# Kernel optimization log

Hardware: AMD Instinct MI355X
Metric: run time of the kernel (lower is better)

Reference implementation:

```python
import jax, jax.numpy as jnp
import numpy as np
import math

N = 50000        # nodes
DEG = 16         # regular out-degree -> E = N*DEG edges, grouped by source node
B = 64           # graphs in batch
F = 128          # num_node_features
H = 128          # nhid == enhid
RATIO = 0.5      # edge_ratio
NUM_CONVS = 3
E = N * DEG


def setup_inputs() -> dict:
    key = jax.random.key(0)
    ks = jax.random.split(key, 18)
    s = 0.05
    x = jax.random.normal(ks[0], (N, F), jnp.float32)
    edge_src = jnp.repeat(jnp.arange(N, dtype=jnp.int32), DEG)          # sorted by src
    edge_dst = jax.random.randint(ks[1], (E,), 0, N, jnp.int32)
    batch = ((jnp.arange(N) * B) // N).astype(jnp.int32)                 # sorted graph ids
    edge_attr = jnp.ones((E, 1), jnp.float32)                            # edge_attr=None branch
    inp = {"x": x, "edge_attr": edge_attr, "edge_src": edge_src,
           "edge_dst": edge_dst, "batch": batch}
    # GCNConv weights: [F->H, H->H, H->H]
    inp["W_gcn0"] = jax.random.normal(ks[2], (F, H), jnp.float32) * s
    inp["b_gcn0"] = jnp.zeros((H,), jnp.float32)
    inp["W_gcn1"] = jax.random.normal(ks[3], (H, H), jnp.float32) * s
    inp["b_gcn1"] = jnp.zeros((H,), jnp.float32)
    inp["W_gcn2"] = jax.random.normal(ks[4], (H, H), jnp.float32) * s
    inp["b_gcn2"] = jnp.zeros((H,), jnp.float32)
    # EGNN edge convs: [1->H, H->H]
    inp["W_eg0"] = jax.random.normal(ks[5], (1, H), jnp.float32) * s
    inp["b_eg0"] = jnp.zeros((H,), jnp.float32)
    inp["W_eg1"] = jax.random.normal(ks[6], (H, H), jnp.float32) * s
    inp["b_eg1"] = jnp.zeros((H,), jnp.float32)
    # score convs: [H->1, H->1]
    inp["W_sc0"] = jax.random.normal(ks[7], (H, 1), jnp.float32) * s
    inp["b_sc0"] = jnp.zeros((1,), jnp.float32)
    inp["W_sc1"] = jax.random.normal(ks[8], (H, 1), jnp.float32) * s
    inp["b_sc1"] = jnp.zeros((1,), jnp.float32)
    return inp


def _gcn(x, src, dst, ew, W, b):
    # PyG GCNConv: add self-loops (weight 1), symmetric deg normalization, aggregate at dst.
    n = x.shape[0]
    loop = jnp.arange(n, dtype=src.dtype)
    src2 = jnp.concatenate([src, loop])
    dst2 = jnp.concatenate([dst, loop])
    ew2 = jnp.concatenate([ew, jnp.ones((n,), ew.dtype)])
    deg = jax.ops.segment_sum(ew2, dst2, n)
    dinv = jnp.where(deg > 0, jax.lax.rsqrt(jnp.maximum(deg, 1e-12)), 0.0)
    norm = dinv[src2] * dinv[dst2] * ew2                                  # [E+n]
    msg = (x @ W)[src2] * norm[:, None]                                    # gather + scale
    return jax.ops.segment_sum(msg, dst2, n) + b                           # scatter-add


def _egnn(e, src, W, b):
    # Edge conv: scatter edge features to their source node, gather back, linear map.
    agg = jax.ops.segment_sum(e, src, N)
    return agg[src] @ W + b


def _pool(h, batch):
    gmax = jax.ops.segment_max(h, batch, B)
    gsum = jax.ops.segment_sum(h, batch, B)
    cnt = jax.ops.segment_sum(jnp.ones((h.shape[0],), h.dtype), batch, B)
    gmean = gsum / cnt[:, None]
    return jnp.concatenate([gmax, gmean, gsum], axis=1)                    # [B, 3H]


def reference(x, edge_attr, edge_src, edge_dst, batch,
              W_gcn0, b_gcn0, W_gcn1, b_gcn1, W_gcn2, b_gcn2,
              W_eg0, b_eg0, W_eg1, b_eg1, W_sc0, b_sc0, W_sc1, b_sc1):
    gW = [W_gcn0, W_gcn1, W_gcn2]
    gb = [b_gcn0, b_gcn1, b_gcn2]
    eW = [W_eg0, W_eg1]
    eb = [b_eg0, b_eg1]
    sW = [W_sc0, W_sc1]
    sb = [b_sc0, b_sc1]
    src, dst = edge_src, edge_dst
    deg = DEG
    ew = jnp.ones((src.shape[0],), jnp.float32)
    h = x
    ea = edge_attr
    xs = jnp.zeros((B, 3 * H), jnp.float32)
    for i in range(NUM_CONVS):
        h = jax.nn.relu(_gcn(h, src, dst, ew, gW[i], gb[i]))
        if i < NUM_CONVS - 1:
            ea = jax.nn.relu(_egnn(ea, src, eW[i], eb[i]))
            score = jnp.tanh(_egnn(ea, src, sW[i], sb[i])[:, 0])           # [E_cur]
            k = math.ceil(RATIO * deg)                                      # per-src-node top-k
            vals, idx = jax.lax.top_k(score.reshape(N, deg), k)             # [N,k]
            dst = jnp.take_along_axis(dst.reshape(N, deg), idx, axis=1).reshape(-1)
            flat = (jnp.arange(N)[:, None] * deg + idx).reshape(-1)
            ea = ea[flat]
            src = jnp.repeat(jnp.arange(N, dtype=src.dtype), k)
            ew = jnp.clip(vals.reshape(-1), 0.0, 1.0)
            deg = k
        xs = xs + _pool(h, batch)
    return xs
```

## Files before the change

### kernel.cpp

```cpp
#include <hip/hip_runtime.h>
#include <math.h>

#define NNODES 50000
#define DEGREE 16
#define NGRAPH 64
#define CAP 64
#define LDA 136
#define NXCD 8
#define XRANGE (NNODES / NXCD)
#define NTILE 782

typedef unsigned short u16;
typedef unsigned int u32;
typedef unsigned long long u64;
using short8 = __attribute__((ext_vector_type(8))) short;
using f32x4  = __attribute__((ext_vector_type(4))) float;
using u16x4  = __attribute__((ext_vector_type(4))) unsigned short;

__device__ __forceinline__ u16 f2bf(float f) {
  union { float f; u32 u; } v; v.f = f;
  u32 u = v.u;
  return (u16)((u + 0x7FFFu + ((u >> 16) & 1u)) >> 16);
}
__device__ __forceinline__ float2 bf2x2(u32 u) {
  union { u32 u; float f; } lo, hi;
  lo.u = (u & 0xFFFFu) << 16; hi.u = u & 0xFFFF0000u;
  return make_float2(lo.f, hi.f);
}
__device__ __forceinline__ u32 pack2(float x, float y) {
  return (u32)f2bf(x) | ((u32)f2bf(y) << 16);
}
__device__ __forceinline__ int lowerb(const int* b, int n, int v) {
  int lo = 0, hi = n;
  while (lo < hi) { int m = (lo + hi) >> 1; if (b[m] < v) lo = m + 1; else hi = m; }
  return lo;
}

__global__ __launch_bounds__(256) void k_init(
    const float* __restrict__ eattr, const float* __restrict__ x,
    const float* __restrict__ weg, const float* __restrict__ beg,
    const float* __restrict__ wsc, const float* __restrict__ bsc,
    const float* __restrict__ W0, const float* __restrict__ W1,
    const float* __restrict__ W2, const float* __restrict__ W3,
    float* __restrict__ ew1, float* __restrict__ agg0,
    u16* __restrict__ xb, u16* __restrict__ Wt,
    const int* __restrict__ edst, int* __restrict__ cnt,
    int* __restrict__ slots) {
  int b = blockIdx.x, t = threadIdx.x;
  if (b < 6250) {
    int i = b * 256 + t;
    float4 v = reinterpret_cast<const float4*>(x)[i];
    u16x4 o = {f2bf(v.x), f2bf(v.y), f2bf(v.z), f2bf(v.w)};
    reinterpret_cast<u16x4*>(xb)[i] = o;
    if (i < NNODES) {
      const float4* p = reinterpret_cast<const float4*>(eattr + (size_t)i * DEGREE);
      float s = 0.f;
#pragma unroll
      for (int j = 0; j < 4; ++j) { float4 w = p[j]; s += w.x + w.y + w.z + w.w; }
      agg0[i] = s;
      float sc = 0.f;
      for (int k = 0; k < 128; ++k) {
        float e = fmaxf(fmaf(s, weg[k], beg[k]), 0.f);
        sc = fmaf(e, wsc[k], sc);
      }
      float v1 = tanhf(fmaf(16.f, sc, bsc[0]));
      ew1[i] = fminf(fmaxf(v1, 0.f), 1.f);
    }
  } else if (b < 6506) {
    int idx = (b - 6250) * 256 + t;
    int which = idx >> 14, r = idx & 16383;
    int k = r >> 7, n = r & 127;
    const float* W = which == 0 ? W0 : which == 1 ? W1 : which == 2 ? W2 : W3;
    Wt[which * 16384 + n * 128 + k] = f2bf(W[k * 128 + n]);
  } else {
    int kk = b - 6506;
    int r = kk & (NXCD - 1);
    int bi = kk >> 3;
    int rlo = r * XRANGE, rhi = rlo + XRANGE;
    int tid = bi * 256 + t;
    for (int e = tid; e < NNODES * DEGREE; e += 128 * 256) {
      int d = edst[e];
      if (d >= rlo && d < rhi) {
        int pos = atomicAdd(&cnt[d], 1);
        if (pos < CAP) slots[(size_t)d * CAP + pos] = e;
      }
    }
  }
}

__global__ __launch_bounds__(256) void k_gemmF(
    int nGemm, const u16* __restrict__ A, const u16* __restrict__ WtA,
    u16* __restrict__ outA,
    int nEg, const float* __restrict__ agg0, const float* __restrict__ weg,
    const float* __restrict__ beg, const u16* __restrict__ WtE,
    const float* __restrict__ beE, const float* __restrict__ wsc1,
    const float* __restrict__ bs1, float* __restrict__ ewOut) {
  __shared__ u16 Bs[128 * LDA];
  __shared__ u16 As[64 * LDA];
  int b = blockIdx.x, t = threadIdx.x;
  int eg = (b >= nGemm);
  const u16* Wsrc = eg ? WtE : WtA;
  for (int i = t; i < 2048; i += 256) {
    int r = i >> 4, c = (i & 15) << 3;
    *reinterpret_cast<uint4*>(&Bs[r * LDA + c]) =
        *reinterpret_cast<const uint4*>(&Wsrc[r * 128 + c]);
  }
  int m0 = (eg ? (b - nGemm) : b) * 64;
  if (eg) {
    for (int idx = t; idx < 64 * 128; idx += 256) {
      int r = idx >> 7, k = idx & 127;
      int row = m0 + r;
      float a = (row < NNODES) ? agg0[row] : 0.f;
      float v = 8.f * fmaxf(fmaf(a, weg[k], beg[k]), 0.f);
      As[r * LDA + k] = f2bf(v);
    }
  } else {
    for (int i = t; i < 1024; i += 256) {
      int r = i >> 4, c = (i & 15) << 3;
      int row = m0 + r;
      uint4 v = make_uint4(0u, 0u, 0u, 0u);
      if (row < NNODES) v = *reinterpret_cast<const uint4*>(&A[(size_t)row * 128 + c]);
      *reinterpret_cast<uint4*>(&As[r * LDA + c]) = v;
    }
  }
  __syncthreads();
  int wave = t >> 6, lane = t & 63;
  int lm = lane & 15, quad = lane >> 4;
  f32x4 z = {0.f, 0.f, 0.f, 0.f};
  f32x4 acc[8];
#pragma unroll
  for (int n = 0; n < 8; ++n) acc[n] = z;
  const u16* arow = &As[(wave * 16 + lm) * LDA + quad * 8];
#pragma unroll
  for (int kc = 0; kc < 4; ++kc) {
    short8 af = *reinterpret_cast<const short8*>(arow + kc * 32);
#pragma unroll
    for (int n = 0; n < 8; ++n) {
      short8 bf = *reinterpret_cast<const short8*>(
          &Bs[(n * 16 + lm) * LDA + kc * 32 + quad * 8]);
      acc[n] = __builtin_amdgcn_mfma_f32_16x16x32_bf16(af, bf, acc[n], 0, 0, 0);
    }
  }
  if (!eg) {
#pragma unroll
    for (int n = 0; n < 8; ++n) {
      int col = n * 16 + lm;
#pragma unroll
      for (int r = 0; r < 4; ++r) {
        int row = m0 + wave * 16 + quad * 4 + r;
        if (row < NNODES) outA[(size_t)row * 128 + col] = f2bf(acc[n][r]);
      }
    }
  } else {
    float s0 = 0.f, s1 = 0.f, s2 = 0.f, s3 = 0.f;
#pragma unroll
    for (int n = 0; n < 8; ++n) {
      int col = n * 16 + lm;
      float bb = beE[col], wv = wsc1[col];
      s0 = fmaf(fmaxf(acc[n][0] + bb, 0.f), wv, s0);
      s1 = fmaf(fmaxf(acc[n][1] + bb, 0.f), wv, s1);
      s2 = fmaf(fmaxf(acc[n][2] + bb, 0.f), wv, s2);
      s3 = fmaf(fmaxf(acc[n][3] + bb, 0.f), wv, s3);
    }
#pragma unroll
    for (int m = 8; m >= 1; m >>= 1) {
      s0 += __shfl_xor(s0, m, 64);
      s1 += __shfl_xor(s1, m, 64);
      s2 += __shfl_xor(s2, m, 64);
      s3 += __shfl_xor(s3, m, 64);
    }
    if (lm == 0) {
      float bsv = bs1[0];
      float sv[4] = {s0, s1, s2, s3};
#pragma unroll
      for (int r = 0; r < 4; ++r) {
        int row = m0 + wave * 16 + quad * 4 + r;
        if (row < NNODES) {
          float v = tanhf(fmaf(8.f, sv[r], bsv));
          ewOut[row] = fminf(fmaxf(v, 0.f), 1.f);
        }
      }
    }
  }
}

__global__ __launch_bounds__(256) void k_small(
    int nDinv, const int* __restrict__ cnt, const int* __restrict__ slots,
    const float* __restrict__ ewIn, float* __restrict__ dinv,
    float* __restrict__ wsrc, int keep,
    const u16* __restrict__ h, const int* __restrict__ batch,
    float* __restrict__ pmax, float* __restrict__ psum) {
  __shared__ float P[16 * 64];
  int b = blockIdx.x, t = threadIdx.x;
  if (b < nDinv) {
    int n = (b * 256 + t) >> 6;
    int lane = t & 63;
    if (n < NNODES) {
      int c = min(cnt[n], CAP);
      u32 ent = 0;
      if (lane < c) ent = (u32)slots[(size_t)n * CAP + lane];
      float e = (lane < c && (ent & 15u) < (u32)keep) ? ewIn[ent >> 4] : 0.f;
#pragma unroll
      for (int m = 32; m >= 1; m >>= 1) e += __shfl_xor(e, m, 64);
      float d = rsqrtf(1.0f + e);
      if (lane == 0) { dinv[n] = d; wsrc[n] = d * ewIn[n]; }
    }
  } else {
    int pb = b - nDinv;
    int g = pb >> 4, sl = pb & 15;
    int lo = lowerb(batch, NNODES, g);
    int hi = lowerb(batch, NNODES, g + 1);
    int len = hi - lo;
    int start = lo + (len * sl) / 16;
    int end = lo + (len * (sl + 1)) / 16;
    int lane = t & 63, rg = t >> 6;
    const u32* hb = reinterpret_cast<const u32*>(h);
    float mxx = 0.f, mxy = 0.f, smx = 0.f, smy = 0.f;
    for (int n = start + rg; n < end; n += 4) {
      float2 v = bf2x2(hb[(size_t)n * 64 + lane]);
      mxx = fmaxf(mxx, v.x); mxy = fmaxf(mxy, v.y);
      smx += v.x; smy += v.y;
    }
    P[(rg * 4 + 0) * 64 + lane] = mxx;
    P[(rg * 4 + 1) * 64 + lane] = mxy;
    P[(rg * 4 + 2) * 64 + lane] = smx;
    P[(rg * 4 + 3) * 64 + lane] = smy;
    __syncthreads();
    if (t < 64) {
      float amx = 0.f, amy = 0.f, asx = 0.f, asy = 0.f;
#pragma unroll
      for (int rgi = 0; rgi < 4; ++rgi) {
        amx = fmaxf(amx, P[(rgi * 4 + 0) * 64 + t]);
        amy = fmaxf(amy, P[(rgi * 4 + 1) * 64 + t]);
        asx += P[(rgi * 4 + 2) * 64 + t];
        asy += P[(rgi * 4 + 3) * 64 + t];
      }
      pmax[(size_t)pb * 128 + 2 * t]     = amx;
      pmax[(size_t)pb * 128 + 2 * t + 1] = amy;
      psum[(size_t)pb * 128 + 2 * t]     = asx;
      psum[(size_t)pb * 128 + 2 * t + 1] = asy;
    }
  }
}

__global__ __launch_bounds__(256) void k_aggp(
    int nAgg, const u16* __restrict__ xwb, const int* __restrict__ cnt,
    const int* __restrict__ slots, const float* __restrict__ wsrc,
    const float* __restrict__ dinv, const float* __restrict__ bias,
    u16* __restrict__ hout, int keep, int l0mode,
    const float* __restrict__ pmax, const float* __restrict__ psum,
    const int* __restrict__ batch, float* __restrict__ out, int poolAdd) {
  int b = blockIdx.x, t = threadIdx.x;
  if (b < nAgg) {
    int n = (b * 256 + t) >> 6;
    int lane = t & 63;
    if (n >= NNODES) return;
    int c = min(cnt[n], CAP);
    u32 e = 0;
    if (lane < c) e = (u32)slots[(size_t)n * CAP + lane];
    int kc; u32 ce;
    if (keep < 16) {
      bool valid = (lane < c) && ((e & 15u) < (u32)keep);
      u64 mask = __ballot(valid);
      kc = (int)__popcll(mask);
      u64 lt = ((u64)1 << lane) - 1;
      int pos = valid ? (int)__popcll(mask & lt) : 63 - (int)__popcll((~mask) & lt);
      ce = (u32)__builtin_amdgcn_ds_permute(pos << 2, (int)e);
    } else { kc = c; ce = e; }
    int sl = 0; float wl = 0.f;
    if (lane < kc) {
      sl = (int)(ce >> 4);
      wl = l0mode ? rsqrtf(1.0f + (float)min(cnt[sl], CAP)) : wsrc[sl];
    }
    const u32* base = reinterpret_cast<const u32*>(xwb);
    float2 acc = make_float2(0.f, 0.f);
    int i = 0;
    for (; i + 8 <= kc; i += 8) {
      u32 r[8]; float w[8];
#pragma unroll
      for (int j = 0; j < 8; ++j) {
        int s = __shfl(sl, i + j, 64);
        w[j] = __shfl(wl, i + j, 64);
        r[j] = base[(size_t)s * 64 + lane];
      }
#pragma unroll
      for (int j = 0; j < 8; ++j) {
        float2 v = bf2x2(r[j]);
        acc.x = fmaf(w[j], v.x, acc.x);
        acc.y = fmaf(w[j], v.y, acc.y);
      }
    }
    for (; i + 4 <= kc; i += 4) {
      u32 r[4]; float w[4];
#pragma unroll
      for (int j = 0; j < 4; ++j) {
        int s = __shfl(sl, i + j, 64);
        w[j] = __shfl(wl, i + j, 64);
        r[j] = base[(size_t)s * 64 + lane];
      }
#pragma unroll
      for (int j = 0; j < 4; ++j) {
        float2 v = bf2x2(r[j]);
        acc.x = fmaf(w[j], v.x, acc.x);
        acc.y = fmaf(w[j], v.y, acc.y);
      }
    }
    for (; i < kc; ++i) {
      int s = __shfl(sl, i, 64);
      float w = __shfl(wl, i, 64);
      float2 v = bf2x2(base[(size_t)s * 64 + lane]);
      acc.x = fmaf(w, v.x, acc.x);
      acc.y = fmaf(w, v.y, acc.y);
    }
    float di = l0mode ? rsqrtf(1.0f + (float)c) : dinv[n];
    float2 self = bf2x2(base[(size_t)n * 64 + lane]);
    float2 bv = reinterpret_cast<const float2*>(bias)[lane];
    float rx = fmaxf(fmaf(di, acc.x, fmaf(di * di, self.x, bv.x)), 0.f);
    float ry = fmaxf(fmaf(di, acc.y, fmaf(di * di, self.y, bv.y)), 0.f);
    reinterpret_cast<u32*>(hout + (size_t)n * 128)[lane] = pack2(rx, ry);
  } else {
    int g = b - nAgg;
    if (t >= 128) return;
    int f = t;
    float mx = 0.f, sm = 0.f;
    for (int s = 0; s < 16; ++s) {
      mx = fmaxf(mx, pmax[(size_t)(g * 16 + s) * 128 + f]);
      sm += psum[(size_t)(g * 16 + s) * 128 + f];
    }
    int lo = lowerb(batch, NNODES, g);
    int hi = lowerb(batch, NNODES, g + 1);
    float cf = (float)(hi - lo);
    float* og = out + g * 384;
    if (poolAdd) {
      og[f] += mx; og[128 + f] += sm / cf; og[256 + f] += sm;
    } else {
      og[f] = mx;  og[128 + f] = sm / cf;  og[256 + f] = sm;
    }
  }
}

extern "C" void kernel_launch(void* const* d_in, const int* in_sizes, int n_in,
                              void* d_out, int out_size, void* d_ws, size_t ws_size,
                              hipStream_t stream) {
  const float* x     = (const float*)d_in[0];
  const float* eattr = (const float*)d_in[1];
  const int*   edst  = (const int*)d_in[3];
  const int*   batch = (const int*)d_in[4];
  const float* Wg0 = (const float*)d_in[5];  const float* bg0 = (const float*)d_in[6];
  const float* Wg1 = (const float*)d_in[7];  const float* bg1 = (const float*)d_in[8];
  const float* Wg2 = (const float*)d_in[9];  const float* bg2 = (const float*)d_in[10];
  const float* We0 = (const float*)d_in[11]; const float* be0 = (const float*)d_in[12];
  const float* We1 = (const float*)d_in[13]; const float* be1 = (const float*)d_in[14];
  const float* Ws0 = (const float*)d_in[15]; const float* bs0 = (const float*)d_in[16];
  const float* Ws1 = (const float*)d_in[17]; const float* bs1 = (const float*)d_in[18];
  float* out = (float*)d_out;

  char* ws = (char*)d_ws;
  const size_t NBH = (size_t)NNODES * 128 * 2;
  size_t off = 0;
  auto alloc = [&](size_t bytes) { void* p = ws + off; off = (off + bytes + 255) & ~(size_t)255; return p; };
  u16*   Xb    = (u16*)alloc(NBH);
  u16*   XWb   = (u16*)alloc(NBH);
  u16*   Hb    = (u16*)alloc(NBH);
  u16*   Wtb   = (u16*)alloc(4 * 128 * 128 * 2);
  int*   slots = (int*)alloc((size_t)NNODES * CAP * 4);
  int*   cnt   = (int*)alloc((size_t)NNODES * 4);
  float* agg0  = (float*)alloc((size_t)NNODES * 4);
  float* ew1   = (float*)alloc((size_t)NNODES * 4);
  float* ew2   = (float*)alloc((size_t)NNODES * 4);
  float* dinv  = (float*)alloc((size_t)NNODES * 4);
  float* wsrc  = (float*)alloc((size_t)NNODES * 4);
  float* pmax  = (float*)alloc((size_t)NGRAPH * 16 * 128 * 4);
  float* psum  = (float*)alloc((size_t)NGRAPH * 16 * 128 * 4);

  hipMemsetAsync(cnt, 0, (size_t)NNODES * 4, stream);
  k_init<<<7530, 256, 0, stream>>>(eattr, x, We0, be0, Ws0, bs0,
                                   Wg0, Wg1, Wg2, We1, ew1, agg0, Xb, Wtb,
                                   edst, cnt, slots);
  k_gemmF<<<2 * NTILE, 256, 0, stream>>>(
      NTILE, Xb, Wtb, XWb,
      NTILE, agg0, We0, be0, Wtb + 3 * 16384, be1, Ws1, bs1, ew2);
  k_aggp<<<12500, 256, 0, stream>>>(12500, XWb, cnt, slots, nullptr, nullptr, bg0,
                                    Hb, 16, 1, nullptr, nullptr, nullptr, nullptr, 0);
  k_small<<<12500 + 1024, 256, 0, stream>>>(12500, cnt, slots, ew1, dinv, wsrc, 8,
                                            Hb, batch, pmax, psum);
  k_gemmF<<<NTILE, 256, 0, stream>>>(
      NTILE, Hb, Wtb + 16384, XWb,
      0, nullptr, nullptr, nullptr, nullptr, nullptr, nullptr, nullptr, nullptr);
  k_aggp<<<12500 + NGRAPH, 256, 0, stream>>>(12500, XWb, cnt, slots, wsrc, dinv, bg1,
                                             Hb, 8, 0, pmax, psum, batch, out, 0);
  k_small<<<12500 + 1024, 256, 0, stream>>>(12500, cnt, slots, ew2, dinv, wsrc, 4,
                                            Hb, batch, pmax, psum);
  k_gemmF<<<NTILE, 256, 0, stream>>>(
      NTILE, Hb, Wtb + 2 * 16384, XWb,
      0, nullptr, nullptr, nullptr, nullptr, nullptr, nullptr, nullptr, nullptr);
  k_aggp<<<12500 + NGRAPH, 256, 0, stream>>>(12500, XWb, cnt, slots, wsrc, dinv, bg2,
                                             Hb, 4, 0, pmax, psum, batch, out, 1);
  k_small<<<1024, 256, 0, stream>>>(0, nullptr, nullptr, nullptr, nullptr, nullptr, 0,
                                    Hb, batch, pmax, psum);
  k_aggp<<<NGRAPH, 256, 0, stream>>>(0, nullptr, nullptr, nullptr, nullptr, nullptr,
                                     nullptr, nullptr, 0, 0, pmax, psum, batch, out, 1);
}
```

Measured before the change: 337.8 us.

## Merge aggregation, dinv and pooling into one node kernel with deferred pooling

Replaces the separate aggregation and small kernels with a single k_node kernel that does the GCN aggregation and can also compute both later layers' degree normalisations, since those depend only on edge scores already available after the first GEMM. Each graph's pooling is now done by a single block and deferred one layer, running alongside the next aggregation on a separate H buffer. This removes the pmax/psum partial buffers and cuts the launch count from 11 to 8. In exchange, the pooling work is spread over 64 blocks instead of 1024, and extra H and dinv buffers are needed.

New measurement: 460.2 us. 1.36x slower.

```diff
diff --git a/kernel.cpp b/kernel.cpp
--- a/kernel.cpp
+++ b/kernel.cpp
@@ -184,76 +184,22 @@
   }
 }
 
-__global__ __launch_bounds__(256) void k_small(
-    int nDinv, const int* __restrict__ cnt, const int* __restrict__ slots,
-    const float* __restrict__ ewIn, float* __restrict__ dinv,
-    float* __restrict__ wsrc, int keep,
-    const u16* __restrict__ h, const int* __restrict__ batch,
-    float* __restrict__ pmax, float* __restrict__ psum) {
+__global__ __launch_bounds__(256) void k_node(
+    int nAgg, const u16* __restrict__ xwb, const int* __restrict__ cnt,
+    const int* __restrict__ slots, const float* __restrict__ wsrcA,
+    const float* __restrict__ dinvA, const float* __restrict__ bias,
+    u16* __restrict__ hout, int keep, int l0mode,
+    int nD1, const float* __restrict__ ewB, float* __restrict__ dinvB,
+    float* __restrict__ wsrcB, int keepB,
+    int nD2, const float* __restrict__ ewC, float* __restrict__ dinvC,
+    float* __restrict__ wsrcC, int keepC,
+    int nPool, const u16* __restrict__ hpool, const int* __restrict__ batch,
+    float* __restrict__ out, int poolAdd) {
   __shared__ float P[16 * 64];
   int b = blockIdx.x, t = threadIdx.x;
-  if (b < nDinv) {
-    int n = (b * 256 + t) >> 6;
-    int lane = t & 63;
-    if (n < NNODES) {
-      int c = min(cnt[n], CAP);
-      u32 ent = 0;
-      if (lane < c) ent = (u32)slots[(size_t)n * CAP + lane];
-      float e = (lane < c && (ent & 15u) < (u32)keep) ? ewIn[ent >> 4] : 0.f;
-#pragma unroll
-      for (int m = 32; m >= 1; m >>= 1) e += __shfl_xor(e, m, 64);
-      float d = rsqrtf(1.0f + e);
-      if (lane == 0) { dinv[n] = d; wsrc[n] = d * ewIn[n]; }
-    }
-  } else {
-    int pb = b - nDinv;
-    int g = pb >> 4, sl = pb & 15;
-    int lo = lowerb(batch, NNODES, g);
-    int hi = lowerb(batch, NNODES, g + 1);
-    int len = hi - lo;
-    int start = lo + (len * sl) / 16;
-    int end = lo + (len * (sl + 1)) / 16;
-    int lane = t & 63, rg = t >> 6;
-    const u32* hb = reinterpret_cast<const u32*>(h);
-    float mxx = 0.f, mxy = 0.f, smx = 0.f, smy = 0.f;
-    for (int n = start + rg; n < end; n += 4) {
-      float2 v = bf2x2(hb[(size_t)n * 64 + lane]);
-      mxx = fmaxf(mxx, v.x); mxy = fmaxf(mxy, v.y);
-      smx += v.x; smy += v.y;
-    }
-    P[(rg * 4 + 0) * 64 + lane] = mxx;
-    P[(rg * 4 + 1) * 64 + lane] = mxy;
-    P[(rg * 4 + 2) * 64 + lane] = smx;
-    P[(rg * 4 + 3) * 64 + lane] = smy;
-    __syncthreads();
-    if (t < 64) {
-      float amx = 0.f, amy = 0.f, asx = 0.f, asy = 0.f;
-#pragma unroll
-      for (int rgi = 0; rgi < 4; ++rgi) {
-        amx = fmaxf(amx, P[(rgi * 4 + 0) * 64 + t]);
-        amy = fmaxf(amy, P[(rgi * 4 + 1) * 64 + t]);
-        asx += P[(rgi * 4 + 2) * 64 + t];
-        asy += P[(rgi * 4 + 3) * 64 + t];
-      }
-      pmax[(size_t)pb * 128 + 2 * t]     = amx;
-      pmax[(size_t)pb * 128 + 2 * t + 1] = amy;
-      psum[(size_t)pb * 128 + 2 * t]     = asx;
-      psum[(size_t)pb * 128 + 2 * t + 1] = asy;
-    }
-  }
-}
-
-__global__ __launch_bounds__(256) void k_aggp(
-    int nAgg, const u16* __restrict__ xwb, const int* __restrict__ cnt,
-    const int* __restrict__ slots, const float* __restrict__ wsrc,
-    const float* __restrict__ dinv, const float* __restrict__ bias,
-    u16* __restrict__ hout, int keep, int l0mode,
-    const float* __restrict__ pmax, const float* __restrict__ psum,
-    const int* __restrict__ batch, float* __restrict__ out, int poolAdd) {
-  int b = blockIdx.x, t = threadIdx.x;
+  int lane = t & 63;
   if (b < nAgg) {
     int n = (b * 256 + t) >> 6;
-    int lane = t & 63;
     if (n >= NNODES) return;
     int c = min(cnt[n], CAP);
     u32 e = 0;
@@ -270,7 +216,7 @@
     int sl = 0; float wl = 0.f;
     if (lane < kc) {
       sl = (int)(ce >> 4);
-      wl = l0mode ? rsqrtf(1.0f + (float)min(cnt[sl], CAP)) : wsrc[sl];
+      wl = l0mode ? rsqrtf(1.0f + (float)min(cnt[sl], CAP)) : wsrcA[sl];
     }
     const u32* base = reinterpret_cast<const u32*>(xwb);
     float2 acc = make_float2(0.f, 0.f);
@@ -312,29 +258,68 @@
       acc.x = fmaf(w, v.x, acc.x);
       acc.y = fmaf(w, v.y, acc.y);
     }
-    float di = l0mode ? rsqrtf(1.0f + (float)c) : dinv[n];
+    float di = l0mode ? rsqrtf(1.0f + (float)c) : dinvA[n];
     float2 self = bf2x2(base[(size_t)n * 64 + lane]);
     float2 bv = reinterpret_cast<const float2*>(bias)[lane];
     float rx = fmaxf(fmaf(di, acc.x, fmaf(di * di, self.x, bv.x)), 0.f);
     float ry = fmaxf(fmaf(di, acc.y, fmaf(di * di, self.y, bv.y)), 0.f);
     reinterpret_cast<u32*>(hout + (size_t)n * 128)[lane] = pack2(rx, ry);
+  } else if (b < nAgg + nD1 + nD2) {
+    int d1 = (b < nAgg + nD1);
+    int idx = d1 ? (b - nAgg) : (b - nAgg - nD1);
+    const float* ew = d1 ? ewB : ewC;
+    float* dv = d1 ? dinvB : dinvC;
+    float* wv = d1 ? wsrcB : wsrcC;
+    int kp = d1 ? keepB : keepC;
+    int n = (idx * 256 + t) >> 6;
+    if (n < NNODES) {
+      int c = min(cnt[n], CAP);
+      u32 ent = 0;
+      if (lane < c) ent = (u32)slots[(size_t)n * CAP + lane];
+      float e = (lane < c && (ent & 15u) < (u32)kp) ? ew[ent >> 4] : 0.f;
+#pragma unroll
+      for (int m = 32; m >= 1; m >>= 1) e += __shfl_xor(e, m, 64);
+      float d = rsqrtf(1.0f + e);
+      if (lane == 0) { dv[n] = d; wv[n] = d * ew[n]; }
+    }
   } else {
-    int g = b - nAgg;
-    if (t >= 128) return;
-    int f = t;
-    float mx = 0.f, sm = 0.f;
-    for (int s = 0; s < 16; ++s) {
-      mx = fmaxf(mx, pmax[(size_t)(g * 16 + s) * 128 + f]);
-      sm += psum[(size_t)(g * 16 + s) * 128 + f];
-    }
+    int g = b - nAgg - nD1 - nD2;
     int lo = lowerb(batch, NNODES, g);
     int hi = lowerb(batch, NNODES, g + 1);
-    float cf = (float)(hi - lo);
-    float* og = out + g * 384;
-    if (poolAdd) {
-      og[f] += mx; og[128 + f] += sm / cf; og[256 + f] += sm;
-    } else {
-      og[f] = mx;  og[128 + f] = sm / cf;  og[256 + f] = sm;
+    int rg = t >> 6;
+    const u32* hb = reinterpret_cast<const u32*>(hpool);
+    float mxx = 0.f, mxy = 0.f, smx = 0.f, smy = 0.f;
+    for (int n = lo + rg; n < hi; n += 4) {
+      float2 v = bf2x2(hb[(size_t)n * 64 + lane]);
+      mxx = fmaxf(mxx, v.x); mxy = fmaxf(mxy, v.y);
+      smx += v.x; smy += v.y;
+    }
+    P[(rg * 4 + 0) * 64 + lane] = mxx;
+    P[(rg * 4 + 1) * 64 + lane] = mxy;
+    P[(rg * 4 + 2) * 64 + lane] = smx;
+    P[(rg * 4 + 3) * 64 + lane] = smy;
+    __syncthreads();
+    if (t < 64) {
+      float amx = 0.f, amy = 0.f, asx = 0.f, asy = 0.f;
+#pragma unroll
+      for (int rgi = 0; rgi < 4; ++rgi) {
+        amx = fmaxf(amx, P[(rgi * 4 + 0) * 64 + t]);
+        amy = fmaxf(amy, P[(rgi * 4 + 1) * 64 + t]);
+        asx += P[(rgi * 4 + 2) * 64 + t];
+        asy += P[(rgi * 4 + 3) * 64 + t];
+      }
+      float cf = (float)(hi - lo);
+      int f0 = 2 * t;
+      float* og = out + g * 384;
+      if (poolAdd) {
+        og[f0] += amx;             og[f0 + 1] += amy;
+        og[128 + f0] += asx / cf;  og[128 + f0 + 1] += asy / cf;
+        og[256 + f0] += asx;       og[256 + f0 + 1] += asy;
+      } else {
+        og[f0] = amx;              og[f0 + 1] = amy;
+        og[128 + f0] = asx / cf;   og[128 + f0 + 1] = asy / cf;
+        og[256 + f0] = asx;        og[256 + f0 + 1] = asy;
+      }
     }
   }
 }
@@ -361,17 +346,19 @@
   auto alloc = [&](size_t bytes) { void* p = ws + off; off = (off + bytes + 255) & ~(size_t)255; return p; };
   u16*   Xb    = (u16*)alloc(NBH);
   u16*   XWb   = (u16*)alloc(NBH);
-  u16*   Hb    = (u16*)alloc(NBH);
+  u16*   Hb0   = (u16*)alloc(NBH);
+  u16*   Hb1   = (u16*)alloc(NBH);
+  u16*   Hb2   = (u16*)alloc(NBH);
   u16*   Wtb   = (u16*)alloc(4 * 128 * 128 * 2);
   int*   slots = (int*)alloc((size_t)NNODES * CAP * 4);
   int*   cnt   = (int*)alloc((size_t)NNODES * 4);
   float* agg0  = (float*)alloc((size_t)NNODES * 4);
   float* ew1   = (float*)alloc((size_t)NNODES * 4);
   float* ew2   = (float*)alloc((size_t)NNODES * 4);
-  float* dinv  = (float*)alloc((size_t)NNODES * 4);
-  float* wsrc  = (float*)alloc((size_t)NNODES * 4);
-  float* pmax  = (float*)alloc((size_t)NGRAPH * 16 * 128 * 4);
-  float* psum  = (float*)alloc((size_t)NGRAPH * 16 * 128 * 4);
+  float* dinv1 = (float*)alloc((size_t)NNODES * 4);
+  float* wsrc1 = (float*)alloc((size_t)NNODES * 4);
+  float* dinv2 = (float*)alloc((size_t)NNODES * 4);
+  float* wsrc2 = (float*)alloc((size_t)NNODES * 4);
 
   hipMemsetAsync(cnt, 0, (size_t)NNODES * 4, stream);
   k_init<<<7530, 256, 0, stream>>>(eattr, x, We0, be0, Ws0, bs0,
@@ -380,24 +367,30 @@
   k_gemmF<<<2 * NTILE, 256, 0, stream>>>(
       NTILE, Xb, Wtb, XWb,
       NTILE, agg0, We0, be0, Wtb + 3 * 16384, be1, Ws1, bs1, ew2);
-  k_aggp<<<12500, 256, 0, stream>>>(12500, XWb, cnt, slots, nullptr, nullptr, bg0,
-                                    Hb, 16, 1, nullptr, nullptr, nullptr, nullptr, 0);
-  k_small<<<12500 + 1024, 256, 0, stream>>>(12500, cnt, slots, ew1, dinv, wsrc, 8,
-                                            Hb, batch, pmax, psum);
+  k_node<<<3 * 12500, 256, 0, stream>>>(
+      12500, XWb, cnt, slots, nullptr, nullptr, bg0, Hb0, 16, 1,
+      12500, ew1, dinv1, wsrc1, 8,
+      12500, ew2, dinv2, wsrc2, 4,
+      0, nullptr, nullptr, nullptr, 0);
   k_gemmF<<<NTILE, 256, 0, stream>>>(
-      NTILE, Hb, Wtb + 16384, XWb,
+      NTILE, Hb0, Wtb + 16384, XWb,
       0, nullptr, nullptr, nullptr, nullptr, nullptr, nullptr, nullptr, nullptr);
-  k_aggp<<<12500 + NGRAPH, 256, 0, stream>>>(12500, XWb, cnt, slots, wsrc, dinv, bg1,
-                                             Hb, 8, 0, pmax, psum, batch, out, 0);
-  k_small<<<12500 + 1024, 256, 0, stream>>>(12500, cnt, slots, ew2, dinv, wsrc, 4,
-                                            Hb, batch, pmax, psum);
+  k_node<<<12500 + NGRAPH, 256, 0, stream>>>(
+      12500, XWb, cnt, slots, wsrc1, dinv1, bg1, Hb1, 8, 0,
+      0, nullptr, nullptr, nullptr, 0,
+      0, nullptr, nullptr, nullptr, 0,
+      NGRAPH, Hb0, batch, out, 0);
   k_gemmF<<<NTILE, 256, 0, stream>>>(
-      NTILE, Hb, Wtb + 2 * 16384, XWb,
+      NTILE, Hb1, Wtb + 2 * 16384, XWb,
       0, nullptr, nullptr, nullptr, nullptr, nullptr, nullptr, nullptr, nullptr);
-  k_aggp<<<12500 + NGRAPH, 256, 0, stream>>>(12500, XWb, cnt, slots, wsrc, dinv, bg2,
-                                             Hb, 4, 0, pmax, psum, batch, out, 1);
-  k_small<<<1024, 256, 0, stream>>>(0, nullptr, nullptr, nullptr, nullptr, nullptr, 0,
-                                    Hb, batch, pmax, psum);
-  k_aggp<<<NGRAPH, 256, 0, stream>>>(0, nullptr, nullptr, nullptr, nullptr, nullptr,
-                                     nullptr, nullptr, 0, 0, pmax, psum, batch, out, 1);
-}
+  k_node<<<12500 + NGRAPH, 256, 0, stream>>>(
+      12500, XWb, cnt, slots, wsrc2, dinv2, bg2, Hb2, 4, 0,
+      0, nullptr, nullptr, nullptr, 0,
+      0, nullptr, nullptr, nullptr, 0,
+      NGRAPH, Hb1, batch, out, 1);
+  k_node<<<NGRAPH, 256, 0, stream>>>(
+      0, nullptr, nullptr, nullptr, nullptr, nullptr, nullptr, nullptr, 0, 0,
+      0, nullptr, nullptr, nullptr, 0,
+      0, nullptr, nullptr, nullptr, 0,
+      NGRAPH, Hb2, batch, out, 1);
+}
```
